# Kernel tuning notes

Measured on AMD Instinct MI355X. Metric: run time of the kernel, lower is better.

Reference implementation:

```python
import jax, jax.numpy as jnp
import numpy as np

KS = 3        # kernel_size
DIL = 2       # dilation
HEAD_DIM = 32


def _unfold(x, ks, dil):
    """torch nn.Unfold(ks, dilation=dil, padding=dil*(ks-1)//2, stride=1).
    x: [B, C, H, W] -> [B, C, ks*ks, H, W] (channel-major patch order, matching torch)."""
    B, C, H, W = x.shape
    pad = dil * (ks - 1) // 2
    xp = jnp.pad(x, ((0, 0), (0, 0), (pad, pad), (pad, pad)))
    pats = [xp[:, :, i * dil:i * dil + H, j * dil:j * dil + W]
            for i in range(ks) for j in range(ks)]
    return jnp.stack(pats, axis=2)


def setup_inputs() -> dict:
    key = jax.random.key(0)
    k1, k2, k3 = jax.random.split(key, 3)
    shape = (16, 128, 64, 64)  # [B, d, H, W]
    return {
        "q": jax.random.normal(k1, shape, dtype=jnp.float32),
        "k": jax.random.normal(k2, shape, dtype=jnp.float32),
        "v": jax.random.normal(k3, shape, dtype=jnp.float32),
    }


def reference(q, k, v):
    B, d, H, W = q.shape
    heads = d // HEAD_DIM
    scale = HEAD_DIM ** (-0.5)
    KK = KS * KS
    # q: [B, heads, head_dim, H*W]
    qr = q.reshape(B, heads, HEAD_DIM, H * W)
    # unfolded k/v: [B, heads, head_dim, KK, H*W]
    ku = _unfold(k, KS, DIL).reshape(B, heads, HEAD_DIM, KK, H * W)
    vu = _unfold(v, KS, DIL).reshape(B, heads, HEAD_DIM, KK, H * W)
    # per-pixel small attention over KK local dilated keys
    attn = jnp.einsum('bhdn,bhdkn->bhnk', qr, ku) * scale  # [B,heads,HW,KK]
    attn = jax.nn.softmax(attn, axis=-1)  # attn_drop = 0 -> identity
    out = jnp.einsum('bhnk,bhdkn->bnhd', attn, vu)  # [B,HW,heads,head_dim]
    return out.reshape(B, H, W, d)
```

## Files before the change

### kernel.cpp

```cpp
#include <hip/hip_runtime.h>

namespace {
constexpr int B = 16, C = 128, H = 64, W = 64;
constexpr int HEADS = 4, HD = 32;
constexpr float SCALE = 0.17677669529663687f;

__global__ __launch_bounds__(256, 4) void dilate_attn(
    const float* __restrict__ q, const float* __restrict__ k,
    const float* __restrict__ v, float* __restrict__ out) {
  __shared__ float4 smem[64 * 32];

  const int tid  = threadIdx.x;
  const int w    = tid & 63;
  const int head = tid >> 6;

  const int blk  = blockIdx.x;
  const int slot = ((blk & 7) << 7) | (blk >> 3);
  const int b    = slot >> 6;
  const int h    = slot & 63;

  const size_t plane = (size_t)H * W;
  const size_t cbase = ((size_t)b * C + head * HD) * plane;
  const float* qp = q + cbase + (size_t)h * W + w;
  const float* kp = k + cbase;
  const float* vp = v + cbase;

  int   offs[9];
  float mask[9];
  #pragma unroll
  for (int iy = 0; iy < 3; ++iy) {
    #pragma unroll
    for (int jx = 0; jx < 3; ++jx) {
      const int kk = iy * 3 + jx;
      const int hh = h + 2 * (iy - 1);
      const int ww = w + 2 * (jx - 1);
      const bool ok = ((unsigned)hh < (unsigned)H) && ((unsigned)ww < (unsigned)W);
      offs[kk] = ok ? hh * W + ww : 0;
      mask[kk] = ok ? 1.0f : 0.0f;
    }
  }

  float l[9];
  #pragma unroll
  for (int kk = 0; kk < 9; ++kk) l[kk] = 0.0f;

  #pragma unroll
  for (int dg = 0; dg < 8; ++dg) {
    float qd[4], kd[4][9];
    #pragma unroll
    for (int di = 0; di < 4; ++di) {
      const int d = dg * 4 + di;
      qd[di] = qp[d * plane];
      const float* kc = kp + d * plane;
      #pragma unroll
      for (int kk = 0; kk < 9; ++kk) kd[di][kk] = kc[offs[kk]];
    }
    #pragma unroll
    for (int di = 0; di < 4; ++di)
      #pragma unroll
      for (int kk = 0; kk < 9; ++kk) l[kk] = fmaf(qd[di], kd[di][kk], l[kk]);
  }

  float m = -1e30f;
  #pragma unroll
  for (int kk = 0; kk < 9; ++kk) {
    l[kk] *= mask[kk];
    m = fmaxf(m, l[kk]);
  }
  float p[9], s = 0.0f;
  #pragma unroll
  for (int kk = 0; kk < 9; ++kk) {
    p[kk] = __expf((l[kk] - m) * SCALE);
    s += p[kk];
  }
  const float r = 1.0f / s;
  #pragma unroll
  for (int kk = 0; kk < 9; ++kk) p[kk] *= r * mask[kk];

  #pragma unroll
  for (int dg = 0; dg < 8; ++dg) {
    float vd[4][9];
    #pragma unroll
    for (int di = 0; di < 4; ++di) {
      const float* vc = vp + (dg * 4 + di) * plane;
      #pragma unroll
      for (int kk = 0; kk < 9; ++kk) vd[di][kk] = vc[offs[kk]];
    }
    float o[4] = {0, 0, 0, 0};
    #pragma unroll
    for (int di = 0; di < 4; ++di)
      #pragma unroll
      for (int kk = 0; kk < 9; ++kk) o[di] = fmaf(p[kk], vd[di][kk], o[di]);

    const int c4 = head * 8 + dg;
    smem[(w << 5) | (c4 ^ (w & 31))] = make_float4(o[0], o[1], o[2], o[3]);
  }

  __syncthreads();

  float4* outp = (float4*)(out + ((size_t)(b * H + h) * W) * C);
  #pragma unroll
  for (int it = 0; it < 8; ++it) {
    const int L = it * 256 + tid;
    const int px = L >> 5, c = L & 31;
    outp[L] = smem[(px << 5) | (c ^ (px & 31))];
  }
}
}

extern "C" void kernel_launch(void* const* d_in, const int* in_sizes, int n_in,
                              void* d_out, int out_size, void* d_ws, size_t ws_size,
                              hipStream_t stream) {
  const float* q = (const float*)d_in[0];
  const float* k = (const float*)d_in[1];
  const float* v = (const float*)d_in[2];
  float* o = (float*)d_out;
  dilate_attn<<<dim3(1024), dim3(256), 0, stream>>>(q, k, v, o);
}
```

Measured before the change: 161.4 us.

## Split head dim across two half-waves with shuffle reduction, double block count

Each block now covers half a row (32 pixels) and the 32 head channels are split across the two halves of a wavefront. The partial attention logits are combined with a cross-lane xor shuffle. This doubles the grid to 2048 blocks, halves per-thread register and shared memory use, and raises launch_bounds occupancy to 8. The goal is more parallelism and latency hiding for a memory-bound gather. The cost is duplicated softmax work in both halves and 32-wide rows, which make narrower coalesced segments.

```diff
diff --git a/kernel.cpp b/kernel.cpp
--- a/kernel.cpp
+++ b/kernel.cpp
@@ -5,22 +5,26 @@
 constexpr int HEADS = 4, HD = 32;
 constexpr float SCALE = 0.17677669529663687f;
 
-__global__ __launch_bounds__(256, 4) void dilate_attn(
+__global__ __launch_bounds__(256, 8) void dilate_attn(
     const float* __restrict__ q, const float* __restrict__ k,
     const float* __restrict__ v, float* __restrict__ out) {
-  __shared__ float4 smem[64 * 32];
+  __shared__ float4 smem[32 * 32];
 
   const int tid  = threadIdx.x;
-  const int w    = tid & 63;
+  const int wl   = tid & 31;
+  const int hf   = (tid >> 5) & 1;
   const int head = tid >> 6;
 
   const int blk  = blockIdx.x;
-  const int slot = ((blk & 7) << 7) | (blk >> 3);
-  const int b    = slot >> 6;
-  const int h    = slot & 63;
+  const int xcd  = blk & 7;
+  const int slot = blk >> 3;
+  const int b    = xcd * 2 + (slot >> 7);
+  const int rh   = slot & 127;
+  const int h    = rh >> 1;
+  const int w    = ((rh & 1) << 5) | wl;
 
   const size_t plane = (size_t)H * W;
-  const size_t cbase = ((size_t)b * C + head * HD) * plane;
+  const size_t cbase = ((size_t)b * C + head * HD + hf * 16) * plane;
   const float* qp = q + cbase + (size_t)h * W + w;
   const float* kp = k + cbase;
   const float* vp = v + cbase;
@@ -46,20 +50,23 @@
 
   #pragma unroll
   for (int dg = 0; dg < 8; ++dg) {
-    float qd[4], kd[4][9];
+    float qd[2], kd[2][9];
     #pragma unroll
-    for (int di = 0; di < 4; ++di) {
-      const int d = dg * 4 + di;
+    for (int di = 0; di < 2; ++di) {
+      const int d = dg * 2 + di;
       qd[di] = qp[d * plane];
       const float* kc = kp + d * plane;
       #pragma unroll
       for (int kk = 0; kk < 9; ++kk) kd[di][kk] = kc[offs[kk]];
     }
     #pragma unroll
-    for (int di = 0; di < 4; ++di)
+    for (int di = 0; di < 2; ++di)
       #pragma unroll
       for (int kk = 0; kk < 9; ++kk) l[kk] = fmaf(qd[di], kd[di][kk], l[kk]);
   }
+
+  #pragma unroll
+  for (int kk = 0; kk < 9; ++kk) l[kk] += __shfl_xor(l[kk], 32, 64);
 
   float m = -1e30f;
   #pragma unroll
@@ -78,32 +85,35 @@
   for (int kk = 0; kk < 9; ++kk) p[kk] *= r * mask[kk];
 
   #pragma unroll
-  for (int dg = 0; dg < 8; ++dg) {
-    float vd[4][9];
-    #pragma unroll
-    for (int di = 0; di < 4; ++di) {
-      const float* vc = vp + (dg * 4 + di) * plane;
-      #pragma unroll
-      for (int kk = 0; kk < 9; ++kk) vd[di][kk] = vc[offs[kk]];
-    }
+  for (int dg4 = 0; dg4 < 4; ++dg4) {
     float o[4] = {0, 0, 0, 0};
     #pragma unroll
-    for (int di = 0; di < 4; ++di)
+    for (int half = 0; half < 2; ++half) {
+      float vd[2][9];
       #pragma unroll
-      for (int kk = 0; kk < 9; ++kk) o[di] = fmaf(p[kk], vd[di][kk], o[di]);
-
-    const int c4 = head * 8 + dg;
-    smem[(w << 5) | (c4 ^ (w & 31))] = make_float4(o[0], o[1], o[2], o[3]);
+      for (int di = 0; di < 2; ++di) {
+        const float* vc = vp + (dg4 * 4 + half * 2 + di) * plane;
+        #pragma unroll
+        for (int kk = 0; kk < 9; ++kk) vd[di][kk] = vc[offs[kk]];
+      }
+      #pragma unroll
+      for (int di = 0; di < 2; ++di)
+        #pragma unroll
+        for (int kk = 0; kk < 9; ++kk)
+          o[half * 2 + di] = fmaf(p[kk], vd[di][kk], o[half * 2 + di]);
+    }
+    const int c4 = head * 8 + hf * 4 + dg4;
+    smem[(wl << 5) | (c4 ^ wl)] = make_float4(o[0], o[1], o[2], o[3]);
   }
 
   __syncthreads();
 
-  float4* outp = (float4*)(out + ((size_t)(b * H + h) * W) * C);
+  float4* outp = (float4*)(out + ((size_t)(b * H + h) * W + ((rh & 1) << 5)) * C);
   #pragma unroll
-  for (int it = 0; it < 8; ++it) {
+  for (int it = 0; it < 4; ++it) {
     const int L = it * 256 + tid;
     const int px = L >> 5, c = L & 31;
-    outp[L] = smem[(px << 5) | (c ^ (px & 31))];
+    outp[L] = smem[(px << 5) | (c ^ px)];
   }
 }
 }
@@ -115,5 +125,5 @@
   const float* k = (const float*)d_in[1];
   const float* v = (const float*)d_in[2];
   float* o = (float*)d_out;
-  dilate_attn<<<dim3(1024), dim3(256), 0, stream>>>(q, k, v, o);
+  dilate_attn<<<dim3(2048), dim3(256), 0, stream>>>(q, k, v, o);
 }
```

After: 216.5 us. +34.2%, slower.

## Vectorize neighbor loads per 4-pixel group and split channels across lanes

Applied to the files above, without the earlier changes.

Each thread now handles 4 adjacent pixels and 8 channels of a head, not 1 pixel and all 32 channels. The dilated 3x3 neighbors are read as three float4 loads per row (left, center, right) and reused across the 4 pixels. Partial QK logits are reduced across the 4 channel quarters with wave shuffles, and the softmax is done in float4 form. This replaces many scalar gathers with vector loads and spreads the channel reduction across lanes, at the cost of shuffle overhead and redundant softmax work in 4 lanes. The block-to-XCD mapping also changes so each XCD covers two batches.

```diff
diff --git a/kernel.cpp b/kernel.cpp
--- a/kernel.cpp
+++ b/kernel.cpp
@@ -1,9 +1,22 @@
 #include <hip/hip_runtime.h>
 
 namespace {
-constexpr int B = 16, C = 128, H = 64, W = 64;
-constexpr int HEADS = 4, HD = 32;
 constexpr float SCALE = 0.17677669529663687f;
+
+__device__ __forceinline__ void fma4(float4& acc, const float4& a,
+                                     float bx, float by, float bz, float bw) {
+  acc.x = fmaf(a.x, bx, acc.x);
+  acc.y = fmaf(a.y, by, acc.y);
+  acc.z = fmaf(a.z, bz, acc.z);
+  acc.w = fmaf(a.w, bw, acc.w);
+}
+__device__ __forceinline__ float4 shflx(const float4& x, int m) {
+  return make_float4(__shfl_xor(x.x, m, 64), __shfl_xor(x.y, m, 64),
+                     __shfl_xor(x.z, m, 64), __shfl_xor(x.w, m, 64));
+}
+__device__ __forceinline__ float getc(const float4& a, int px) {
+  return px == 0 ? a.x : px == 1 ? a.y : px == 2 ? a.z : a.w;
+}
 
 __global__ __launch_bounds__(256, 4) void dilate_attn(
     const float* __restrict__ q, const float* __restrict__ k,
@@ -11,94 +24,134 @@
   __shared__ float4 smem[64 * 32];
 
   const int tid  = threadIdx.x;
-  const int w    = tid & 63;
+  const int pxg  = tid & 15;
+  const int cq   = (tid >> 4) & 3;
   const int head = tid >> 6;
 
   const int blk  = blockIdx.x;
-  const int slot = ((blk & 7) << 7) | (blk >> 3);
-  const int b    = slot >> 6;
+  const int xcd  = blk & 7;
+  const int slot = blk >> 3;
+  const int b    = xcd * 2 + (slot >> 6);
   const int h    = slot & 63;
+  const int w0   = pxg << 2;
 
-  const size_t plane = (size_t)H * W;
-  const size_t cbase = ((size_t)b * C + head * HD) * plane;
-  const float* qp = q + cbase + (size_t)h * W + w;
-  const float* kp = k + cbase;
-  const float* vp = v + cbase;
+  int rowi[3]; float my[3];
+  #pragma unroll
+  for (int dy = 0; dy < 3; ++dy) {
+    const int ry = h + 2 * (dy - 1);
+    const bool ok = (unsigned)ry < 64u;
+    rowi[dy] = (ok ? ry : h) * 64;
+    my[dy] = ok ? 1.0f : 0.0f;
+  }
+  const int   colL  = (pxg == 0)  ? w0 : w0 - 4;
+  const int   colR  = (pxg == 15) ? w0 : w0 + 4;
+  const float mxm01 = (pxg == 0)  ? 0.0f : 1.0f;
+  const float mxp23 = (pxg == 15) ? 0.0f : 1.0f;
 
-  int   offs[9];
-  float mask[9];
+  const size_t cb = ((size_t)b * 128 + head * 32 + cq * 8) * 4096;
+  const float* qb = q + cb + h * 64 + w0;
+  const float* kb = k + cb;
+  const float* vb = v + cb;
+
+  float4 l[9];
   #pragma unroll
-  for (int iy = 0; iy < 3; ++iy) {
+  for (int t = 0; t < 9; ++t) l[t] = make_float4(0.f, 0.f, 0.f, 0.f);
+
+  #pragma unroll
+  for (int c = 0; c < 8; ++c) {
+    const float4 q4 = *(const float4*)(qb + c * 4096);
+    const float* kc = kb + c * 4096;
     #pragma unroll
-    for (int jx = 0; jx < 3; ++jx) {
-      const int kk = iy * 3 + jx;
-      const int hh = h + 2 * (iy - 1);
-      const int ww = w + 2 * (jx - 1);
-      const bool ok = ((unsigned)hh < (unsigned)H) && ((unsigned)ww < (unsigned)W);
-      offs[kk] = ok ? hh * W + ww : 0;
-      mask[kk] = ok ? 1.0f : 0.0f;
+    for (int dy = 0; dy < 3; ++dy) {
+      const float* kr = kc + rowi[dy];
+      const float4 Lv = *(const float4*)(kr + colL);
+      const float4 Cv = *(const float4*)(kr + w0);
+      const float4 Rv = *(const float4*)(kr + colR);
+      fma4(l[dy * 3 + 0], q4, Lv.z, Lv.w, Cv.x, Cv.y);
+      fma4(l[dy * 3 + 1], q4, Cv.x, Cv.y, Cv.z, Cv.w);
+      fma4(l[dy * 3 + 2], q4, Cv.z, Cv.w, Rv.x, Rv.y);
     }
   }
 
-  float l[9];
   #pragma unroll
-  for (int kk = 0; kk < 9; ++kk) l[kk] = 0.0f;
+  for (int t = 0; t < 9; ++t) {
+    float4 a = shflx(l[t], 16);
+    l[t].x += a.x; l[t].y += a.y; l[t].z += a.z; l[t].w += a.w;
+    a = shflx(l[t], 32);
+    l[t].x += a.x; l[t].y += a.y; l[t].z += a.z; l[t].w += a.w;
+  }
 
   #pragma unroll
-  for (int dg = 0; dg < 8; ++dg) {
-    float qd[4], kd[4][9];
-    #pragma unroll
-    for (int di = 0; di < 4; ++di) {
-      const int d = dg * 4 + di;
-      qd[di] = qp[d * plane];
-      const float* kc = kp + d * plane;
-      #pragma unroll
-      for (int kk = 0; kk < 9; ++kk) kd[di][kk] = kc[offs[kk]];
-    }
-    #pragma unroll
-    for (int di = 0; di < 4; ++di)
-      #pragma unroll
-      for (int kk = 0; kk < 9; ++kk) l[kk] = fmaf(qd[di], kd[di][kk], l[kk]);
+  for (int dy = 0; dy < 3; ++dy) {
+    const float m0 = my[dy];
+    l[dy*3+0].x *= m0 * mxm01; l[dy*3+0].y *= m0 * mxm01;
+    l[dy*3+0].z *= m0;         l[dy*3+0].w *= m0;
+    l[dy*3+1].x *= m0; l[dy*3+1].y *= m0; l[dy*3+1].z *= m0; l[dy*3+1].w *= m0;
+    l[dy*3+2].x *= m0;         l[dy*3+2].y *= m0;
+    l[dy*3+2].z *= m0 * mxp23; l[dy*3+2].w *= m0 * mxp23;
   }
 
-  float m = -1e30f;
+  float4 mx = l[0];
   #pragma unroll
-  for (int kk = 0; kk < 9; ++kk) {
-    l[kk] *= mask[kk];
-    m = fmaxf(m, l[kk]);
+  for (int t = 1; t < 9; ++t) {
+    mx.x = fmaxf(mx.x, l[t].x); mx.y = fmaxf(mx.y, l[t].y);
+    mx.z = fmaxf(mx.z, l[t].z); mx.w = fmaxf(mx.w, l[t].w);
   }
-  float p[9], s = 0.0f;
+  float4 s = make_float4(0.f, 0.f, 0.f, 0.f);
   #pragma unroll
-  for (int kk = 0; kk < 9; ++kk) {
-    p[kk] = __expf((l[kk] - m) * SCALE);
-    s += p[kk];
+  for (int t = 0; t < 9; ++t) {
+    l[t].x = __expf((l[t].x - mx.x) * SCALE);
+    l[t].y = __expf((l[t].y - mx.y) * SCALE);
+    l[t].z = __expf((l[t].z - mx.z) * SCALE);
+    l[t].w = __expf((l[t].w - mx.w) * SCALE);
+    s.x += l[t].x; s.y += l[t].y; s.z += l[t].z; s.w += l[t].w;
   }
-  const float r = 1.0f / s;
+  const float4 r = make_float4(1.f / s.x, 1.f / s.y, 1.f / s.z, 1.f / s.w);
   #pragma unroll
-  for (int kk = 0; kk < 9; ++kk) p[kk] *= r * mask[kk];
+  for (int t = 0; t < 9; ++t) {
+    l[t].x *= r.x; l[t].y *= r.y; l[t].z *= r.z; l[t].w *= r.w;
+  }
+  #pragma unroll
+  for (int dy = 0; dy < 3; ++dy) {
+    const float m0 = my[dy];
+    l[dy*3+0].x *= m0 * mxm01; l[dy*3+0].y *= m0 * mxm01;
+    l[dy*3+0].z *= m0;         l[dy*3+0].w *= m0;
+    l[dy*3+1].x *= m0; l[dy*3+1].y *= m0; l[dy*3+1].z *= m0; l[dy*3+1].w *= m0;
+    l[dy*3+2].x *= m0;         l[dy*3+2].y *= m0;
+    l[dy*3+2].z *= m0 * mxp23; l[dy*3+2].w *= m0 * mxp23;
+  }
 
   #pragma unroll
-  for (int dg = 0; dg < 8; ++dg) {
-    float vd[4][9];
+  for (int pc = 0; pc < 2; ++pc) {
+    float4 o[4];
     #pragma unroll
-    for (int di = 0; di < 4; ++di) {
-      const float* vc = vp + (dg * 4 + di) * plane;
+    for (int j = 0; j < 4; ++j) o[j] = make_float4(0.f, 0.f, 0.f, 0.f);
+    #pragma unroll
+    for (int j = 0; j < 4; ++j) {
+      const float* vc = vb + (pc * 4 + j) * 4096;
       #pragma unroll
-      for (int kk = 0; kk < 9; ++kk) vd[di][kk] = vc[offs[kk]];
+      for (int dy = 0; dy < 3; ++dy) {
+        const float* vr = vc + rowi[dy];
+        const float4 Lv = *(const float4*)(vr + colL);
+        const float4 Cv = *(const float4*)(vr + w0);
+        const float4 Rv = *(const float4*)(vr + colR);
+        fma4(o[j], l[dy * 3 + 0], Lv.z, Lv.w, Cv.x, Cv.y);
+        fma4(o[j], l[dy * 3 + 1], Cv.x, Cv.y, Cv.z, Cv.w);
+        fma4(o[j], l[dy * 3 + 2], Cv.z, Cv.w, Rv.x, Rv.y);
+      }
     }
-    float o[4] = {0, 0, 0, 0};
+    const int c4 = head * 8 + cq * 2 + pc;
     #pragma unroll
-    for (int di = 0; di < 4; ++di)
-      #pragma unroll
-      for (int kk = 0; kk < 9; ++kk) o[di] = fmaf(p[kk], vd[di][kk], o[di]);
-
-    const int c4 = head * 8 + dg;
-    smem[(w << 5) | (c4 ^ (w & 31))] = make_float4(o[0], o[1], o[2], o[3]);
+    for (int px = 0; px < 4; ++px) {
+      const int pg = w0 + px;
+      smem[(pg << 5) | (c4 ^ (pg & 31))] =
+          make_float4(getc(o[0], px), getc(o[1], px), getc(o[2], px), getc(o[3], px));
+    }
   }
 
   __syncthreads();
 
-  float4* outp = (float4*)(out + ((size_t)(b * H + h) * W) * C);
+  float4* outp = (float4*)(out + ((size_t)(b * 64 + h) * 64) * 128);
   #pragma unroll
   for (int it = 0; it < 8; ++it) {
     const int L = it * 256 + tid;
```

Measured after the change: 200.7 us. 1.24x slower.
